# Kernel tuning notes

Hardware: AMD Instinct MI355X
Metric: run time of the kernel (lower is better)

## Reference

```python
import jax, jax.numpy as jnp
import numpy as np
from jax import lax

DG, KH, KW = 8, 3, 3
STRIDE, PAD, DIL = 1, 1, 1


def setup_inputs() -> dict:
    key = jax.random.key(0)
    ks = jax.random.split(key, 6)
    B, C, H, W = 4, 256, 64, 64
    Cout = 256
    off_ch = DG * 3 * KH * KW  # 216
    x = jax.random.normal(ks[0], (B, C, H, W), dtype=jnp.float32)
    extra_feat = jax.random.normal(ks[1], (B, C, H, W), dtype=jnp.float32)
    weight = jax.random.normal(ks[2], (Cout, C, KH, KW), dtype=jnp.float32) * 0.02
    bias = jax.random.normal(ks[3], (Cout,), dtype=jnp.float32) * 0.01
    off_w = jax.random.normal(ks[4], (off_ch, C, KH, KW), dtype=jnp.float32) * 0.01
    off_b = jax.random.normal(ks[5], (off_ch,), dtype=jnp.float32) * 0.01
    return {"x": x, "extra_feat": extra_feat, "weight": weight, "bias": bias,
            "off_w": off_w, "off_b": off_b}


def _modulated_deform_conv(x, offset, mask, weight, bias):
    B, C, H, W = x.shape
    Cout = weight.shape[0]
    K = KH * KW
    Ho, Wo = offset.shape[2], offset.shape[3]
    Cg = C // DG

    # offset: [B, 2*DG*K, Ho, Wo] interpreted as (dg, K, (dy, dx)) interleaved
    off = offset.reshape(B, DG, K, 2, Ho, Wo)
    dy, dx = off[:, :, :, 0], off[:, :, :, 1]  # [B, DG, K, Ho, Wo]

    ky = jnp.repeat(jnp.arange(KH), KW)  # [K]
    kx = jnp.tile(jnp.arange(KW), KH)    # [K]
    base_y = (jnp.arange(Ho) * STRIDE - PAD)[None, None, None, :, None] + (ky * DIL)[None, None, :, None, None]
    base_x = (jnp.arange(Wo) * STRIDE - PAD)[None, None, None, None, :] + (kx * DIL)[None, None, :, None, None]
    py = dy + base_y  # [B, DG, K, Ho, Wo]
    px = dx + base_x

    y0f = jnp.floor(py)
    x0f = jnp.floor(px)
    fy = py - y0f
    fx = px - x0f
    y0 = y0f.astype(jnp.int32)
    x0 = x0f.astype(jnp.int32)

    xg = x.reshape(B, DG, Cg, H * W)
    N = K * Ho * Wo

    def gather(yi, xi):
        valid = ((yi >= 0) & (yi < H) & (xi >= 0) & (xi < W)).astype(x.dtype)
        idx = (jnp.clip(yi, 0, H - 1) * W + jnp.clip(xi, 0, W - 1)).reshape(B, DG, 1, N)
        g = jnp.take_along_axis(xg, jnp.broadcast_to(idx, (B, DG, Cg, N)), axis=-1)
        g = g.reshape(B, DG, Cg, K, Ho, Wo)
        return g * valid[:, :, None]

    val = (((1 - fy) * (1 - fx))[:, :, None] * gather(y0, x0)
           + ((1 - fy) * fx)[:, :, None] * gather(y0, x0 + 1)
           + (fy * (1 - fx))[:, :, None] * gather(y0 + 1, x0)
           + (fy * fx)[:, :, None] * gather(y0 + 1, x0 + 1))
    val = val * mask.reshape(B, DG, 1, K, Ho, Wo)
    val = val.reshape(B, C, K, Ho, Wo)

    out = jnp.einsum('bckhw,ock->bohw', val, weight.reshape(Cout, C, K))
    return out + bias[None, :, None, None]


def reference(x, extra_feat, weight, bias, off_w, off_b):
    # conv_offset: plain conv predicting offsets + mask
    om = lax.conv_general_dilated(
        extra_feat, off_w, window_strides=(STRIDE, STRIDE),
        padding=((PAD, PAD), (PAD, PAD)), rhs_dilation=(DIL, DIL),
        dimension_numbers=('NCHW', 'OIHW', 'NCHW')) + off_b[None, :, None, None]
    o1, o2, mask = jnp.split(om, 3, axis=1)
    offset = jnp.concatenate([o1, o2], axis=1)
    mask = jax.nn.sigmoid(mask)
    return _modulated_deform_conv(x, offset, mask, weight, bias)
```

## Files before the change

kernel.cpp:

```cpp
#include <hip/hip_runtime.h>
#include <hip/hip_bf16.h>
#include <math.h>

#define BB 4
#define CC 256
#define HH 64
#define WW 64
#define HW 4096
#define PH 68
#define PW 68
#define COUT 256
#define OFFC 216
#define KTOT 2304
#define NCHUNK 72

typedef __attribute__((ext_vector_type(4))) float f32x4;
typedef __attribute__((ext_vector_type(8))) short s16x8;
typedef __attribute__((ext_vector_type(8))) unsigned short u16x8;
typedef __attribute__((ext_vector_type(2))) unsigned int u32x2;
typedef __attribute__((ext_vector_type(4))) unsigned int u32x4;

__device__ __forceinline__ unsigned short f2bf(float f) {
    unsigned int u = __float_as_uint(f);
    return (unsigned short)((u + 0x7fffu + ((u >> 16) & 1u)) >> 16);
}
__device__ __forceinline__ float bflo(unsigned int u) { return __uint_as_float(u << 16); }
__device__ __forceinline__ float bfhi(unsigned int u) { return __uint_as_float(u & 0xffff0000u); }
__device__ __forceinline__ unsigned int pkbf(float a, float b) {
    __hip_bfloat162 h = __float22bfloat162_rn(make_float2(a, b));
    unsigned int r;
    __builtin_memcpy(&r, &h, 4);
    return r;
}

#define WAITL() asm volatile("s_waitcnt lgkmcnt(0)" ::: "memory")
#define RBAR() __builtin_amdgcn_s_barrier()

__global__ __launch_bounds__(256) void pack_w_main(const float* __restrict__ w,
                                                   unsigned short* __restrict__ wp) {
    int idx = blockIdx.x * 256 + threadIdx.x;
    int t = idx >> 13, r = idx & 8191;
    int oc = r >> 5, s = (r >> 3) & 3, e = r & 7;
    int kk = ((s ^ ((oc >> 1) & 3)) << 3) | e;
    int dg = t / 9, tap = t - dg * 9;
    int c = dg * 32 + kk;
    wp[idx] = f2bf(w[((size_t)oc * CC + c) * 9 + tap]);
}

__global__ __launch_bounds__(256) void pack_w_off(const float* __restrict__ w,
                                                  unsigned short* __restrict__ wp) {
    int idx = blockIdx.x * 256 + threadIdx.x;
    int t = idx >> 13, r = idx & 8191;
    int oc = r >> 5, s = (r >> 3) & 3, e = r & 7;
    int kk = ((s ^ ((oc >> 1) & 3)) << 3) | e;
    int tap = t >> 3, cg = t & 7;
    int c = cg * 32 + kk;
    float v = (oc < OFFC) ? w[((size_t)oc * CC + c) * 9 + tap] : 0.f;
    wp[idx] = f2bf(v);
}

__global__ __launch_bounds__(256) void pad_tr2(const float* __restrict__ srcx,
                                               const float* __restrict__ srce,
                                               unsigned short* __restrict__ dx_,
                                               unsigned short* __restrict__ de_) {
    const float* src = blockIdx.y ? srce : srcx;
    unsigned short* dst = blockIdx.y ? de_ : dx_;
    int blk = blockIdx.x;
    int b = blk / PH, yp = blk % PH;
    int y = yp - 2;
    unsigned short* drow = dst + ((size_t)b * PH + yp) * PW * CC;
    int tid = threadIdx.x;
    if ((unsigned)y >= (unsigned)HH) {
        for (int i = tid; i < PW * CC / 8; i += 256) *(u16x8*)&drow[(size_t)i * 8] = (u16x8)0;
        return;
    }
    __shared__ float tile[64][65];
    int lane = tid & 63, w = tid >> 6;
    int oct = tid & 7, xi = tid >> 3;
    const float* srow = src + (size_t)b * CC * HW + (size_t)y * WW;
    for (int chunk = 0; chunk < 4; chunk++) {
        __syncthreads();
#pragma unroll
        for (int i = 0; i < 16; i++) {
            int c = chunk * 64 + w * 16 + i;
            tile[w * 16 + i][lane] = srow[(size_t)c * HW + lane];
        }
        __syncthreads();
#pragma unroll
        for (int xq = 0; xq < 3; xq++) {
            int xp = xq * 32 + xi;
            if (xp < PW) {
                int x = xp - 2;
                u16x8 v = (u16x8)0;
                if ((unsigned)x < (unsigned)WW) {
#pragma unroll
                    for (int e = 0; e < 8; e++) v[e] = f2bf(tile[oct * 8 + e][x]);
                }
                *(u16x8*)&drow[(size_t)xp * CC + chunk * 64 + oct * 8] = v;
            }
        }
    }
}


#define A_LOAD(WPP, T, AF)                                                \
    {                                                                     \
        const unsigned short* wt_ = WPP + (size_t)(T) * 8192 + aoff;      \
        AF[0] = *(const s16x8*)&wt_[0];                                   \
        AF[1] = *(const s16x8*)&wt_[512];                                 \
        AF[2] = *(const s16x8*)&wt_[8192];                                \
        AF[3] = *(const s16x8*)&wt_[8704];                                \
    }

#define MFMA8R(AC, BUF)                                                                      \
    {                                                                                        \
        int sw_ = (lg ^ ((r16 >> 1) & 3)) << 3;                                              \
        s16x8 b0_ = *(const s16x8*)&sB[BUF][0][r16 * 32 + sw_];                              \
        s16x8 b1_ = *(const s16x8*)&sB[BUF][0][(16 + r16) * 32 + sw_];                       \
        acc[0][0] = __builtin_amdgcn_mfma_f32_16x16x32_bf16(AC[0], b0_, acc[0][0], 0, 0, 0); \
        acc[0][1] = __builtin_amdgcn_mfma_f32_16x16x32_bf16(AC[0], b1_, acc[0][1], 0, 0, 0); \
        acc[1][0] = __builtin_amdgcn_mfma_f32_16x16x32_bf16(AC[1], b0_, acc[1][0], 0, 0, 0); \
        acc[1][1] = __builtin_amdgcn_mfma_f32_16x16x32_bf16(AC[1], b1_, acc[1][1], 0, 0, 0); \
        b0_ = *(const s16x8*)&sB[BUF][1][r16 * 32 + sw_];                                    \
        b1_ = *(const s16x8*)&sB[BUF][1][(16 + r16) * 32 + sw_];                             \
        acc[0][0] = __builtin_amdgcn_mfma_f32_16x16x32_bf16(AC[2], b0_, acc[0][0], 0, 0, 0); \
        acc[0][1] = __builtin_amdgcn_mfma_f32_16x16x32_bf16(AC[2], b1_, acc[0][1], 0, 0, 0); \
        acc[1][0] = __builtin_amdgcn_mfma_f32_16x16x32_bf16(AC[3], b0_, acc[1][0], 0, 0, 0); \
        acc[1][1] = __builtin_amdgcn_mfma_f32_16x16x32_bf16(AC[3], b1_, acc[1][1], 0, 0, 0); \
    }

__global__ __launch_bounds__(512, 4) void off_mfma(const unsigned short* __restrict__ eT,
                                                   const unsigned short* __restrict__ wp,
                                                   const float* __restrict__ off_b,
                                                   float* __restrict__ omP) {
    __shared__ __align__(16) unsigned short sB[2][2][1024];
    __shared__ float sAcc[256 * 33];
    int bx = blockIdx.x;
    int b = bx >> 6, y = bx & 63;
    int pxh = blockIdx.y;
    int tid = threadIdx.x;
    int lane = tid & 63;
    int w = tid >> 6;
    int r16 = lane & 15, lg = lane >> 4;
    int px_l = tid >> 4, ch2 = tid & 15;
    int pxg = pxh * 32 + px_l;
    int aoff = (w * 32 + r16) * 32 + ((lg ^ ((r16 >> 1) & 3)) << 3);

    const unsigned short* eb = eT + (size_t)b * PH * PW * CC;

    f32x4 acc[2][2];
#pragma unroll
    for (int mi = 0; mi < 2; mi++)
#pragma unroll
        for (int ni = 0; ni < 2; ni++) acc[mi][ni] = (f32x4)0.f;

    s16x8 aA[4], aB[4];

#define BSLOT2 (px_l * 32 + ((((ch2 >> 2) ^ ((px_l >> 1) & 3))) << 3) + (ch2 & 3) * 2)
#define OF_B(T, BV)                                                                          \
    {                                                                                        \
        int tap_ = (T) >> 3, cg_ = (T) & 7;                                                  \
        int ky_ = tap_ / 3, kx_ = tap_ - ky_ * 3;                                            \
        BV = *(const unsigned int*)&eb[(size_t)((y + ky_ + 1) * PW + (pxg + kx_ + 1)) * CC + \
                                       cg_ * 32 + ch2 * 2];                                  \
    }
#define OF_ITF(T, BUF, AC, AN, BP0, BP1, BN0, BN1)               \
    {                                                            \
        A_LOAD(wp, (T) + 2, AN)                                  \
        OF_B((T) + 4, BN0)                                       \
        OF_B((T) + 5, BN1)                                       \
        MFMA8R(AC, BUF)                                          \
        *(unsigned int*)&sB[(BUF) ^ 1][0][BSLOT2] = BP0;         \
        *(unsigned int*)&sB[(BUF) ^ 1][1][BSLOT2] = BP1;         \
        WAITL();                                                 \
        RBAR();                                                  \
    }

    unsigned int bP0, bP1, bN0, bN1;
    {
        A_LOAD(wp, 0, aA)
        unsigned int c0, c1;
        OF_B(0, c0)
        OF_B(1, c1)
        *(unsigned int*)&sB[0][0][BSLOT2] = c0;
        *(unsigned int*)&sB[0][1][BSLOT2] = c1;
        OF_B(2, bP0)
        OF_B(3, bP1)
        WAITL();
        RBAR();
    }
    for (int t = 0; t < 68; t += 4) {
        OF_ITF(t, 0, aA, aB, bP0, bP1, bN0, bN1)
        OF_ITF(t + 2, 1, aB, aA, bN0, bN1, bP0, bP1)
    }
    {
        A_LOAD(wp, 70, aB)
        MFMA8R(aA, 0)
        *(unsigned int*)&sB[1][0][BSLOT2] = bP0;
        *(unsigned int*)&sB[1][1][BSLOT2] = bP1;
        WAITL();
        RBAR();
    }
    MFMA8R(aB, 1)

    __syncthreads();
#pragma unroll
    for (int mi = 0; mi < 2; mi++) {
#pragma unroll
        for (int ni = 0; ni < 2; ni++) {
#pragma unroll
            for (int j = 0; j < 4; j++) {
                int oc = w * 32 + mi * 16 + lg * 4 + j;
                float bv = (oc < OFFC) ? off_b[oc] : 0.f;
                sAcc[oc * 33 + ni * 16 + r16] = acc[mi][ni][j] + bv;
            }
        }
    }
    __syncthreads();
    float* omPb = omP + (size_t)b * NCHUNK * HW * 4;
    for (int i = tid; i < NCHUNK * 32; i += 512) {
        int tt = i >> 5, px = i & 31;
        int dg = (tt * 57) >> 9;
        int tap = tt - dg * 9;
        int ky = tap / 3, kx = tap - ky * 3;
        float dyv = sAcc[(dg * 18 + 2 * tap) * 33 + px];
        float dxv = sAcc[(dg * 18 + 2 * tap + 1) * 33 + px];
        float mr = sAcc[(144 + dg * 9 + tap) * 33 + px];
        int xg = pxh * 32 + px;
        float mv = 1.f / (1.f + __expf(-mr));
        float py = (float)(y + ky - 1) + dyv;
        float pxx = (float)(xg + kx - 1) + dxv;
        float y0f = floorf(py), x0f = floorf(pxx);
        float fy = py - y0f, fx = pxx - x0f;
        int yp0 = min(max((int)y0f + 2, 0), PH - 1);
        int yp1 = min(max((int)y0f + 3, 0), PH - 1);
        int xp0 = min(max((int)x0f + 2, 0), PW - 1);
        int xp1 = min(max((int)x0f + 3, 0), PW - 1);
        unsigned int iv = (unsigned int)(yp0 * PW + xp0) | ((unsigned int)(xp1 - xp0) << 13) |
                          ((unsigned int)(yp1 - yp0) << 14);
        float w00 = (1.f - fy) * (1.f - fx) * mv;
        float w01 = (1.f - fy) * fx * mv;
        float w10 = fy * (1.f - fx) * mv;
        float w11 = fy * fx * mv;
        u32x4 o;
        o[0] = iv;
        o[1] = pkbf(w00, w01);
        o[2] = pkbf(w10, w11);
        o[3] = 0;
        *(u32x4*)(omPb + ((size_t)tt * HW + y * WW + xg) * 4) = o;
    }
}

__global__ __launch_bounds__(512, 4) void dconv_mfma(const unsigned short* __restrict__ xT,
                                                     const float* __restrict__ omP,
                                                     const unsigned short* __restrict__ wp,
                                                     const float* __restrict__ bias,
                                                     float* __restrict__ out) {
    __shared__ __align__(16) unsigned short sB[2][2][1024];
    int bx = blockIdx.x;
    int b = bx >> 6, y = bx & 63;
    int pxh = blockIdx.y;
    int tid = threadIdx.x;
    int lane = tid & 63;
    int w = tid >> 6;
    int r16 = lane & 15, lg = lane >> 4;
    int kt = tid >> 8;
    int px_l = (tid >> 3) & 31;
    int ch4 = tid & 7;
    int yx = y * WW + pxh * 32 + px_l;
    int aoff = (w * 32 + r16) * 32 + ((lg ^ ((r16 >> 1) & 3)) << 3);

    const unsigned short* xb = xT + (size_t)b * PH * PW * CC;
    const float* omPb = omP + (size_t)b * NCHUNK * HW * 4;

    f32x4 acc[2][2];
#pragma unroll
    for (int mi = 0; mi < 2; mi++)
#pragma unroll
        for (int ni = 0; ni < 2; ni++) acc[mi][ni] = (f32x4)0.f;

    s16x8 aA[4], aB[4];

#define BSLOT4 (px_l * 32 + ((((ch4 >> 1) ^ ((px_l >> 1) & 3))) << 3) + (ch4 & 1) * 4)
#define DC_OML(T) (*(const u32x4*)(omPb + ((size_t)(T)*HW + yx) * 4))

#define DC_G(T, OM, G00, G01, G10, G11)                                   \
    {                                                                     \
        int dg_ = ((T) * 57) >> 9;                                        \
        unsigned int iv_ = OM[0];                                         \
        int o00_ = (int)(iv_ & 8191u) << 8;                               \
        int dxe_ = (int)((iv_ >> 13) & 1u) << 8;                          \
        int dye_ = ((iv_ >> 14) & 1u) ? (PW * CC) : 0;                    \
        const unsigned short* p_ = xb + dg_ * 32 + ch4 * 4;               \
        G00 = *(const u32x2*)(p_ + o00_);                                 \
        G01 = *(const u32x2*)(p_ + o00_ + dxe_);                          \
        G10 = *(const u32x2*)(p_ + o00_ + dye_);                          \
        G11 = *(const u32x2*)(p_ + o00_ + dye_ + dxe_);                   \
    }
#define DC_FIN(OM, G00, G01, G10, G11, BUF)                                               \
    {                                                                                     \
        float w00 = bflo(OM[1]), w01 = bfhi(OM[1]);                                       \
        float w10 = bflo(OM[2]), w11 = bfhi(OM[2]);                                       \
        float v0 = w00 * bflo(G00[0]) + w01 * bflo(G01[0]) + w10 * bflo(G10[0]) +         \
                   w11 * bflo(G11[0]);                                                    \
        float v1 = w00 * bfhi(G00[0]) + w01 * bfhi(G01[0]) + w10 * bfhi(G10[0]) +         \
                   w11 * bfhi(G11[0]);                                                    \
        float v2 = w00 * bflo(G00[1]) + w01 * bflo(G01[1]) + w10 * bflo(G10[1]) +         \
                   w11 * bflo(G11[1]);                                                    \
        float v3 = w00 * bfhi(G00[1]) + w01 * bfhi(G01[1]) + w10 * bfhi(G10[1]) +         \
                   w11 * bfhi(G11[1]);                                                    \
        u32x2 pk_;                                                                        \
        pk_[0] = pkbf(v0, v1);                                                            \
        pk_[1] = pkbf(v2, v3);                                                            \
        *(u32x2*)&sB[BUF][kt][BSLOT4] = pk_;                                              \
    }
#define DC_ITF(T, BUF, AC, AN, GP0, GP1, GP2, GP3, GN0, GN1, GN2, GN3, SF, SG) \
    {                                                                          \
        A_LOAD(wp, (T) + 2, AN)                                                \
        DC_G((T) + 4 + kt, SG, GN0, GN1, GN2, GN3)                             \
        MFMA8R(AC, BUF)                                                        \
        DC_FIN(SF, GP0, GP1, GP2, GP3, (BUF) ^ 1)                              \
        SF = DC_OML((T) + 6 + kt);                                             \
        WAITL();                                                               \
        RBAR();                                                                \
    }

    u32x4 omA, omB;
    u32x2 gA0, gA1, gA2, gA3, gB0, gB1, gB2, gB3;
    {
        A_LOAD(wp, 0, aA)
        u32x4 om0 = DC_OML(kt);
        omA = DC_OML(2 + kt);
        u32x2 t0, t1, t2, t3;
        DC_G(kt, om0, t0, t1, t2, t3)
        DC_FIN(om0, t0, t1, t2, t3, 0)
        DC_G(2 + kt, omA, gA0, gA1, gA2, gA3)
        omB = DC_OML(4 + kt);
        WAITL();
        RBAR();
    }
    for (int t = 0; t < 64; t += 4) {
        DC_ITF(t, 0, aA, aB, gA0, gA1, gA2, gA3, gB0, gB1, gB2, gB3, omA, omB)
        DC_ITF(t + 2, 1, aB, aA, gB0, gB1, gB2, gB3, gA0, gA1, gA2, gA3, omB, omA)
    }
    DC_ITF(64, 0, aA, aB, gA0, gA1, gA2, gA3, gB0, gB1, gB2, gB3, omA, omB)
    {
        A_LOAD(wp, 68, aA)
        DC_G(70 + kt, omA, gA0, gA1, gA2, gA3)
        MFMA8R(aB, 1)
        DC_FIN(omB, gB0, gB1, gB2, gB3, 0)
        WAITL();
        RBAR();
    }
    {
        A_LOAD(wp, 70, aB)
        MFMA8R(aA, 0)
        DC_FIN(omA, gA0, gA1, gA2, gA3, 1)
        WAITL();
        RBAR();
    }
    MFMA8R(aB, 1)

#pragma unroll
    for (int mi = 0; mi < 2; mi++) {
#pragma unroll
        for (int ni = 0; ni < 2; ni++) {
#pragma unroll
            for (int j = 0; j < 4; j++) {
                int oc = w * 32 + mi * 16 + lg * 4 + j;
                int pxo = pxh * 32 + ni * 16 + r16;
                out[(size_t)(b * COUT + oc) * HW + y * WW + pxo] = acc[mi][ni][j] + bias[oc];
            }
        }
    }
}

extern "C" void kernel_launch(void* const* d_in, const int* in_sizes, int n_in,
                              void* d_out, int out_size, void* d_ws, size_t ws_size,
                              hipStream_t stream) {
    const float* x = (const float*)d_in[0];
    const float* extra_feat = (const float*)d_in[1];
    const float* weight = (const float*)d_in[2];
    const float* bias = (const float*)d_in[3];
    const float* off_w = (const float*)d_in[4];
    const float* off_b = (const float*)d_in[5];
    float* out = (float*)d_out;

    float* omP = (float*)d_ws;
    unsigned short* wpm = (unsigned short*)(omP + (size_t)BB * NCHUNK * HW * 4);
    unsigned short* wpo = wpm + (size_t)KTOT * COUT;
    unsigned short* xT = wpo + (size_t)KTOT * COUT;
    unsigned short* eT = xT + (size_t)BB * PH * PW * CC;

    pack_w_main<<<(KTOT * COUT) / 256, 256, 0, stream>>>(weight, wpm);
    pack_w_off<<<(KTOT * COUT) / 256, 256, 0, stream>>>(off_w, wpo);
    pad_tr2<<<dim3(BB * PH, 2), 256, 0, stream>>>(x, extra_feat, xT, eT);

    off_mfma<<<dim3(BB * HH, 2), 512, 0, stream>>>(eT, wpo, off_b, omP);
    dconv_mfma<<<dim3(BB * HH, 2), 512, 0, stream>>>(xT, omP, wpm, bias, out);
}
```

Measured before the change: 100.4 us.

## Fuse offset conv and deformable conv into one kernel via LDS handoff

Merges the offset/mask convolution kernel and the deformable convolution kernel into a single kernel. The per-pixel sampling indices and bilinear weights now stay in shared memory instead of being written to a global workspace and read back. This removes a large global round trip and one kernel launch. In exchange, each block uses more LDS, which can reduce occupancy, and the two phases can no longer overlap across separate kernels.

```diff
diff --git a/kernel.cpp b/kernel.cpp
--- a/kernel.cpp
+++ b/kernel.cpp
@@ -129,12 +129,17 @@
         acc[1][1] = __builtin_amdgcn_mfma_f32_16x16x32_bf16(AC[3], b1_, acc[1][1], 0, 0, 0); \
     }
 
-__global__ __launch_bounds__(512, 4) void off_mfma(const unsigned short* __restrict__ eT,
-                                                   const unsigned short* __restrict__ wp,
-                                                   const float* __restrict__ off_b,
-                                                   float* __restrict__ omP) {
+__global__ __launch_bounds__(512, 4) void fused_dcn(const unsigned short* __restrict__ eT,
+                                                    const unsigned short* __restrict__ xT,
+                                                    const unsigned short* __restrict__ wpo,
+                                                    const unsigned short* __restrict__ wpm,
+                                                    const float* __restrict__ off_b,
+                                                    const float* __restrict__ bias,
+                                                    float* __restrict__ out) {
     __shared__ __align__(16) unsigned short sB[2][2][1024];
-    __shared__ float sAcc[256 * 33];
+    __shared__ __align__(16) unsigned int prep[NCHUNK][32][3];
+    __shared__ float sAcc[OFFC * 33];
+
     int bx = blockIdx.x;
     int b = bx >> 6, y = bx & 63;
     int pxh = blockIdx.y;
@@ -142,11 +147,15 @@
     int lane = tid & 63;
     int w = tid >> 6;
     int r16 = lane & 15, lg = lane >> 4;
-    int px_l = tid >> 4, ch2 = tid & 15;
-    int pxg = pxh * 32 + px_l;
     int aoff = (w * 32 + r16) * 32 + ((lg ^ ((r16 >> 1) & 3)) << 3);
+    int p1px = tid >> 4, ch2 = tid & 15;
+    int pxg = pxh * 32 + p1px;
+    int kt = tid >> 8;
+    int p2px = (tid >> 3) & 31;
+    int ch4 = tid & 7;
 
     const unsigned short* eb = eT + (size_t)b * PH * PW * CC;
+    const unsigned short* xb = xT + (size_t)b * PH * PW * CC;
 
     f32x4 acc[2][2];
 #pragma unroll
@@ -156,7 +165,7 @@
 
     s16x8 aA[4], aB[4];
 
-#define BSLOT2 (px_l * 32 + ((((ch2 >> 2) ^ ((px_l >> 1) & 3))) << 3) + (ch2 & 3) * 2)
+#define BSLOT2 (p1px * 32 + ((((ch2 >> 2) ^ ((p1px >> 1) & 3))) << 3) + (ch2 & 3) * 2)
 #define OF_B(T, BV)                                                                          \
     {                                                                                        \
         int tap_ = (T) >> 3, cg_ = (T) & 7;                                                  \
@@ -166,7 +175,7 @@
     }
 #define OF_ITF(T, BUF, AC, AN, BP0, BP1, BN0, BN1)               \
     {                                                            \
-        A_LOAD(wp, (T) + 2, AN)                                  \
+        A_LOAD(wpo, (T) + 2, AN)                                 \
         OF_B((T) + 4, BN0)                                       \
         OF_B((T) + 5, BN1)                                       \
         MFMA8R(AC, BUF)                                          \
@@ -176,32 +185,34 @@
         RBAR();                                                  \
     }
 
-    unsigned int bP0, bP1, bN0, bN1;
     {
-        A_LOAD(wp, 0, aA)
-        unsigned int c0, c1;
-        OF_B(0, c0)
-        OF_B(1, c1)
-        *(unsigned int*)&sB[0][0][BSLOT2] = c0;
-        *(unsigned int*)&sB[0][1][BSLOT2] = c1;
-        OF_B(2, bP0)
-        OF_B(3, bP1)
-        WAITL();
-        RBAR();
-    }
-    for (int t = 0; t < 68; t += 4) {
-        OF_ITF(t, 0, aA, aB, bP0, bP1, bN0, bN1)
-        OF_ITF(t + 2, 1, aB, aA, bN0, bN1, bP0, bP1)
-    }
-    {
-        A_LOAD(wp, 70, aB)
-        MFMA8R(aA, 0)
-        *(unsigned int*)&sB[1][0][BSLOT2] = bP0;
-        *(unsigned int*)&sB[1][1][BSLOT2] = bP1;
-        WAITL();
-        RBAR();
-    }
-    MFMA8R(aB, 1)
+        unsigned int bP0, bP1, bN0, bN1;
+        {
+            A_LOAD(wpo, 0, aA)
+            unsigned int c0, c1;
+            OF_B(0, c0)
+            OF_B(1, c1)
+            *(unsigned int*)&sB[0][0][BSLOT2] = c0;
+            *(unsigned int*)&sB[0][1][BSLOT2] = c1;
+            OF_B(2, bP0)
+            OF_B(3, bP1)
+            WAITL();
+            RBAR();
+        }
+        for (int t = 0; t < 68; t += 4) {
+            OF_ITF(t, 0, aA, aB, bP0, bP1, bN0, bN1)
+            OF_ITF(t + 2, 1, aB, aA, bN0, bN1, bP0, bP1)
+        }
+        {
+            A_LOAD(wpo, 70, aB)
+            MFMA8R(aA, 0)
+            *(unsigned int*)&sB[1][0][BSLOT2] = bP0;
+            *(unsigned int*)&sB[1][1][BSLOT2] = bP1;
+            WAITL();
+            RBAR();
+        }
+        MFMA8R(aB, 1)
+    }
 
     __syncthreads();
 #pragma unroll
@@ -211,13 +222,11 @@
 #pragma unroll
             for (int j = 0; j < 4; j++) {
                 int oc = w * 32 + mi * 16 + lg * 4 + j;
-                float bv = (oc < OFFC) ? off_b[oc] : 0.f;
-                sAcc[oc * 33 + ni * 16 + r16] = acc[mi][ni][j] + bv;
+                if (oc < OFFC) sAcc[oc * 33 + ni * 16 + r16] = acc[mi][ni][j] + off_b[oc];
             }
         }
     }
     __syncthreads();
-    float* omPb = omP + (size_t)b * NCHUNK * HW * 4;
     for (int i = tid; i < NCHUNK * 32; i += 512) {
         int tt = i >> 5, px = i & 31;
         int dg = (tt * 57) >> 9;
@@ -236,58 +245,27 @@
         int yp1 = min(max((int)y0f + 3, 0), PH - 1);
         int xp0 = min(max((int)x0f + 2, 0), PW - 1);
         int xp1 = min(max((int)x0f + 3, 0), PW - 1);
-        unsigned int iv = (unsigned int)(yp0 * PW + xp0) | ((unsigned int)(xp1 - xp0) << 13) |
+        prep[tt][px][0] = (unsigned int)(yp0 * PW + xp0) | ((unsigned int)(xp1 - xp0) << 13) |
                           ((unsigned int)(yp1 - yp0) << 14);
         float w00 = (1.f - fy) * (1.f - fx) * mv;
         float w01 = (1.f - fy) * fx * mv;
         float w10 = fy * (1.f - fx) * mv;
         float w11 = fy * fx * mv;
-        u32x4 o;
-        o[0] = iv;
-        o[1] = pkbf(w00, w01);
-        o[2] = pkbf(w10, w11);
-        o[3] = 0;
-        *(u32x4*)(omPb + ((size_t)tt * HW + y * WW + xg) * 4) = o;
-    }
-}
-
-__global__ __launch_bounds__(512, 4) void dconv_mfma(const unsigned short* __restrict__ xT,
-                                                     const float* __restrict__ omP,
-                                                     const unsigned short* __restrict__ wp,
-                                                     const float* __restrict__ bias,
-                                                     float* __restrict__ out) {
-    __shared__ __align__(16) unsigned short sB[2][2][1024];
-    int bx = blockIdx.x;
-    int b = bx >> 6, y = bx & 63;
-    int pxh = blockIdx.y;
-    int tid = threadIdx.x;
-    int lane = tid & 63;
-    int w = tid >> 6;
-    int r16 = lane & 15, lg = lane >> 4;
-    int kt = tid >> 8;
-    int px_l = (tid >> 3) & 31;
-    int ch4 = tid & 7;
-    int yx = y * WW + pxh * 32 + px_l;
-    int aoff = (w * 32 + r16) * 32 + ((lg ^ ((r16 >> 1) & 3)) << 3);
-
-    const unsigned short* xb = xT + (size_t)b * PH * PW * CC;
-    const float* omPb = omP + (size_t)b * NCHUNK * HW * 4;
-
-    f32x4 acc[2][2];
+        prep[tt][px][1] = pkbf(w00, w01);
+        prep[tt][px][2] = pkbf(w10, w11);
+    }
+    __syncthreads();
+
 #pragma unroll
     for (int mi = 0; mi < 2; mi++)
 #pragma unroll
         for (int ni = 0; ni < 2; ni++) acc[mi][ni] = (f32x4)0.f;
 
-    s16x8 aA[4], aB[4];
-
-#define BSLOT4 (px_l * 32 + ((((ch4 >> 1) ^ ((px_l >> 1) & 3))) << 3) + (ch4 & 1) * 4)
-#define DC_OML(T) (*(const u32x4*)(omPb + ((size_t)(T)*HW + yx) * 4))
-
-#define DC_G(T, OM, G00, G01, G10, G11)                                   \
+#define BSLOT4 (p2px * 32 + ((((ch4 >> 1) ^ ((p2px >> 1) & 3))) << 3) + (ch4 & 1) * 4)
+#define DC_G(T, G00, G01, G10, G11)                                       \
     {                                                                     \
         int dg_ = ((T) * 57) >> 9;                                        \
-        unsigned int iv_ = OM[0];                                         \
+        unsigned int iv_ = prep[T][p2px][0];                              \
         int o00_ = (int)(iv_ & 8191u) << 8;                               \
         int dxe_ = (int)((iv_ >> 13) & 1u) << 8;                          \
         int dye_ = ((iv_ >> 14) & 1u) ? (PW * CC) : 0;                    \
@@ -297,10 +275,12 @@
         G10 = *(const u32x2*)(p_ + o00_ + dye_);                          \
         G11 = *(const u32x2*)(p_ + o00_ + dye_ + dxe_);                   \
     }
-#define DC_FIN(OM, G00, G01, G10, G11, BUF)                                               \
+#define DC_FIN(T, G00, G01, G10, G11, BUF)                                                \
     {                                                                                     \
-        float w00 = bflo(OM[1]), w01 = bfhi(OM[1]);                                       \
-        float w10 = bflo(OM[2]), w11 = bfhi(OM[2]);                                       \
+        unsigned int wa_ = prep[T][p2px][1];                                              \
+        unsigned int wb_ = prep[T][p2px][2];                                              \
+        float w00 = bflo(wa_), w01 = bfhi(wa_);                                           \
+        float w10 = bflo(wb_), w11 = bfhi(wb_);                                           \
         float v0 = w00 * bflo(G00[0]) + w01 * bflo(G01[0]) + w10 * bflo(G10[0]) +         \
                    w11 * bflo(G11[0]);                                                    \
         float v1 = w00 * bfhi(G00[0]) + w01 * bfhi(G01[0]) + w10 * bfhi(G10[0]) +         \
@@ -314,52 +294,42 @@
         pk_[1] = pkbf(v2, v3);                                                            \
         *(u32x2*)&sB[BUF][kt][BSLOT4] = pk_;                                              \
     }
-#define DC_ITF(T, BUF, AC, AN, GP0, GP1, GP2, GP3, GN0, GN1, GN2, GN3, SF, SG) \
-    {                                                                          \
-        A_LOAD(wp, (T) + 2, AN)                                                \
-        DC_G((T) + 4 + kt, SG, GN0, GN1, GN2, GN3)                             \
-        MFMA8R(AC, BUF)                                                        \
-        DC_FIN(SF, GP0, GP1, GP2, GP3, (BUF) ^ 1)                              \
-        SF = DC_OML((T) + 6 + kt);                                             \
-        WAITL();                                                               \
-        RBAR();                                                                \
-    }
-
-    u32x4 omA, omB;
-    u32x2 gA0, gA1, gA2, gA3, gB0, gB1, gB2, gB3;
+#define DC_ITF(T, BUF, AC, AN, GP0, GP1, GP2, GP3, GN0, GN1, GN2, GN3)     \
+    {                                                                      \
+        A_LOAD(wpm, (T) + 2, AN)                                           \
+        DC_G((T) + 4 + kt, GN0, GN1, GN2, GN3)                             \
+        MFMA8R(AC, BUF)                                                    \
+        DC_FIN((T) + 2 + kt, GP0, GP1, GP2, GP3, (BUF) ^ 1)                \
+        WAITL();                                                           \
+        RBAR();                                                            \
+    }
+
     {
-        A_LOAD(wp, 0, aA)
-        u32x4 om0 = DC_OML(kt);
-        omA = DC_OML(2 + kt);
-        u32x2 t0, t1, t2, t3;
-        DC_G(kt, om0, t0, t1, t2, t3)
-        DC_FIN(om0, t0, t1, t2, t3, 0)
-        DC_G(2 + kt, omA, gA0, gA1, gA2, gA3)
-        omB = DC_OML(4 + kt);
-        WAITL();
-        RBAR();
-    }
-    for (int t = 0; t < 64; t += 4) {
-        DC_ITF(t, 0, aA, aB, gA0, gA1, gA2, gA3, gB0, gB1, gB2, gB3, omA, omB)
-        DC_ITF(t + 2, 1, aB, aA, gB0, gB1, gB2, gB3, gA0, gA1, gA2, gA3, omB, omA)
-    }
-    DC_ITF(64, 0, aA, aB, gA0, gA1, gA2, gA3, gB0, gB1, gB2, gB3, omA, omB)
-    {
-        A_LOAD(wp, 68, aA)
-        DC_G(70 + kt, omA, gA0, gA1, gA2, gA3)
+        u32x2 gA0, gA1, gA2, gA3, gB0, gB1, gB2, gB3;
+        {
+            A_LOAD(wpm, 0, aA)
+            u32x2 t0, t1, t2, t3;
+            DC_G(kt, t0, t1, t2, t3)
+            DC_FIN(kt, t0, t1, t2, t3, 0)
+            DC_G(2 + kt, gA0, gA1, gA2, gA3)
+            WAITL();
+            RBAR();
+        }
+        for (int t = 0; t < 64; t += 4) {
+            DC_ITF(t, 0, aA, aB, gA0, gA1, gA2, gA3, gB0, gB1, gB2, gB3)
+            DC_ITF(t + 2, 1, aB, aA, gB0, gB1, gB2, gB3, gA0, gA1, gA2, gA3)
+        }
+        DC_ITF(64, 0, aA, aB, gA0, gA1, gA2, gA3, gB0, gB1, gB2, gB3)
+        DC_ITF(66, 1, aB, aA, gB0, gB1, gB2, gB3, gA0, gA1, gA2, gA3)
+        {
+            A_LOAD(wpm, 70, aB)
+            MFMA8R(aA, 0)
+            DC_FIN(70 + kt, gA0, gA1, gA2, gA3, 1)
+            WAITL();
+            RBAR();
+        }
         MFMA8R(aB, 1)
-        DC_FIN(omB, gB0, gB1, gB2, gB3, 0)
-        WAITL();
-        RBAR();
-    }
-    {
-        A_LOAD(wp, 70, aB)
-        MFMA8R(aA, 0)
-        DC_FIN(omA, gA0, gA1, gA2, gA3, 1)
-        WAITL();
-        RBAR();
-    }
-    MFMA8R(aB, 1)
+    }
 
 #pragma unroll
     for (int mi = 0; mi < 2; mi++) {
@@ -386,8 +356,7 @@
     const float* off_b = (const float*)d_in[5];
     float* out = (float*)d_out;
 
-    float* omP = (float*)d_ws;
-    unsigned short* wpm = (unsigned short*)(omP + (size_t)BB * NCHUNK * HW * 4);
+    unsigned short* wpm = (unsigned short*)d_ws;
     unsigned short* wpo = wpm + (size_t)KTOT * COUT;
     unsigned short* xT = wpo + (size_t)KTOT * COUT;
     unsigned short* eT = xT + (size_t)BB * PH * PW * CC;
@@ -396,6 +365,5 @@
     pack_w_off<<<(KTOT * COUT) / 256, 256, 0, stream>>>(off_w, wpo);
     pad_tr2<<<dim3(BB * PH, 2), 256, 0, stream>>>(x, extra_feat, xT, eT);
 
-    off_mfma<<<dim3(BB * HH, 2), 512, 0, stream>>>(eT, wpo, off_b, omP);
-    dconv_mfma<<<dim3(BB * HH, 2), 512, 0, stream>>>(xT, omP, wpm, bias, out);
-}
+    fused_dcn<<<dim3(BB * HH, 2), 512, 0, stream>>>(eT, xT, wpo, wpm, off_b, bias, out);
+}
```

Result: faster. 89.74 us (-10.6%).
